# Optimization experiments

Hardware: AMD Instinct MI355X
Metric: run time of the kernel (lower is better)

## Reference

```python
import jax, jax.numpy as jnp
import numpy as np

VOXEL_SIZE = 0.4
PC_START = jnp.array([-75.2, -75.2], dtype=jnp.float32)
GAMMA = 1.1
RADII = (0.8, 1.6)
NSAMPLES = (16, 32)


def _sq_dist(a, b):
    # a:[N,3], b:[N,3] -> [N,N] squared distances (no [N,N,3] intermediate)
    sa = jnp.sum(a * a, axis=-1)
    sb = jnp.sum(b * b, axis=-1)
    return jnp.maximum(sa[:, None] + sb[None, :] - 2.0 * (a @ b.T), 0.0)


def _ball_group(d2, valid, pts, r, k):
    # CUDA ball_query semantics: first-k in-radius neighbor indices (index order),
    # empty slots padded with the first found index (0 if none).
    N = d2.shape[0]
    mask = (d2 < r * r) & valid[None, :]
    skey = jnp.where(mask, jnp.arange(N, dtype=jnp.int32)[None, :], N)
    idx = jnp.sort(skey, axis=-1)[:, :k]            # [N,k]
    first = idx[:, :1]
    idx = jnp.where(idx == N, first, idx)
    idx = jnp.where(idx == N, 0, idx)
    grouped_xyz = pts[idx, :3] - pts[:, None, :3]   # [N,k,3] relative xyz
    return jnp.concatenate([grouped_xyz, pts[idx, 3:5]], axis=-1)  # [N,k,5] (use_xyz)


def _mlp(x, ws, bs):
    for w, b in zip(ws, bs):
        x = jax.nn.relu(x @ w.T + b)
    return x


def _frame(pts, boxes, mlps, num_sample):
    # pts: [N,5] (x,y,z,intensity,time); boxes: [M,7]
    xy = pts[:, :2]
    coords = jnp.floor((xy - PC_START) / VOXEL_SIZE)              # per-point voxel xy coord
    qcoords = jnp.floor((boxes[:, :2] - PC_START) / VOXEL_SIZE)   # box voxel coords
    half_diag = jnp.linalg.norm(boxes[:, 3:5] * 0.5, axis=-1)
    rad_vox = jnp.ceil(half_diag * GAMMA / VOXEL_SIZE)
    dvox = jnp.abs(qcoords[:, None, :] - coords[None, :, :])      # [M,N,2]
    valid = jnp.any(jnp.all(dvox < rad_vox[:, None, None], axis=-1), axis=0)  # [N]

    # cylindrical_pool: per-box top-k points inside cylinder radius
    cur_radiis = half_diag * GAMMA
    dis = jnp.linalg.norm(boxes[:, None, :2] - xy[None, :, :], axis=-1)  # [M,N]
    point_mask = (dis <= cur_radiis[:, None]) & valid[None, :]
    sampled_mask, sampled_idx = jax.lax.top_k(point_mask.astype(pts.dtype), num_sample)

    # PointNet++ SA-MSG evaluated at every point (equivalent to unique->gather in torch src)
    d2 = _sq_dist(pts[:, :3], pts[:, :3])
    feats = [pts[:, :3]]  # use_absolute_xyz: concat query xyz first
    for r, k, (ws, bs) in zip(RADII, NSAMPLES, mlps):
        g = _ball_group(d2, valid, pts, r, k)
        feats.append(jnp.max(_mlp(g, ws, bs), axis=1))  # max-pool over neighbors
    feats = jnp.concatenate(feats, axis=-1)             # [N, 3+32+64]

    sampled_points = pts[sampled_idx] * sampled_mask[..., None]  # zero out-of-radius slots
    return sampled_points, feats[sampled_idx]


def _forward(points, trajectory_rois, params, num_sample):
    B, T, N, C = points.shape
    M = trajectory_rois.shape[2]
    sp, pf = jax.vmap(lambda p, b: _frame(p, b, params, num_sample))(
        points.reshape(B * T, N, C), trajectory_rois.reshape(B * T, M, -1))

    def _merge(x):
        x = x.reshape(B, T, M, num_sample, x.shape[-1])
        return x.transpose(0, 2, 1, 3, 4).reshape(B, M, T * num_sample, x.shape[-1])

    return _merge(sp), _merge(pf)


def setup_inputs():
    key = jax.random.key(0)
    ks = jax.random.split(key, 24)
    B, T, N, M = 2, 4, 4096, 128
    xy = jax.random.uniform(ks[0], (B, T, N, 2), minval=-74.0, maxval=74.0)
    z = jax.random.uniform(ks[1], (B, T, N, 1), minval=-2.0, maxval=4.0)
    inten = jax.random.uniform(ks[2], (B, T, N, 1))
    ts = jnp.broadcast_to(jnp.arange(T, dtype=jnp.float32)[None, :, None, None] * 0.1, (B, T, N, 1))
    points = jnp.concatenate([xy, z, inten, ts], axis=-1)
    bxy = jax.random.uniform(ks[3], (B, T, M, 2), minval=-70.0, maxval=70.0)
    bz = jax.random.uniform(ks[4], (B, T, M, 1), minval=-1.0, maxval=1.0)
    bdxy = jax.random.uniform(ks[5], (B, T, M, 2), minval=1.5, maxval=5.0)
    bdz = jax.random.uniform(ks[6], (B, T, M, 1), minval=1.0, maxval=2.0)
    bh = jax.random.uniform(ks[7], (B, T, M, 1), minval=0.0, maxval=6.28)
    trajectory_rois = jnp.concatenate([bxy, bz, bdxy, bdz, bh], axis=-1)
    inp = {"points": points, "trajectory_rois": trajectory_rois}
    dims = [("w00", 16, 5), ("w01", 16, 16), ("w02", 32, 16),
            ("w10", 32, 5), ("w11", 32, 32), ("w12", 64, 32)]
    for i, (nm, o, ic) in enumerate(dims):
        inp[nm] = jax.random.normal(ks[8 + i], (o, ic), dtype=jnp.float32) / np.sqrt(ic)
        inp["b" + nm[1:]] = jnp.zeros((o,), dtype=jnp.float32)
    inp["num_sample"] = 32
    return inp


def reference(points, trajectory_rois, w00, b00, w01, b01, w02, b02,
              w10, b10, w11, b11, w12, b12, num_sample):
    params = (((w00, w01, w02), (b00, b01, b02)),
              ((w10, w11, w12), (b10, b11, b12)))
    return _forward(points, trajectory_rois, params, num_sample)
```

## Files before the change

### kernel.cpp

```cpp
#include <hip/hip_runtime.h>
#include <hip/hip_bf16.h>
#include <stdint.h>

#define NFRM 8
#define NPTS 4096
#define NBOX 128
#define NS   32
#define TT   4
#define BB   2
#define FEATC 99
#define OUT1OFF (BB*NBOX*TT*NS*5)

#define WS_SPK    0u
#define WS_EPK    524288u
#define WS_FEATS  786432u
#define WS_SIDX   13762560u
#define WS_FLAGS  13893632u
#define WS_NCNT   14024704u
#define WS_NLST   14024736u
#define WS_VPK    14155808u
#define WS_VEK    14680096u
#define WS_VORIG  14942240u
#define WS_VCNT   15073312u
#define WS_WT     15073344u

__device__ __forceinline__ float rdl(float x, int l){
    return __int_as_float(__builtin_amdgcn_readlane(__float_as_int(x), l));
}

__global__ void k_wprep(const float* __restrict__ w00,const float* __restrict__ w01,
                        const float* __restrict__ w02,const float* __restrict__ w10,
                        const float* __restrict__ w11,const float* __restrict__ w12,
                        float* __restrict__ wt)
{
    int t = threadIdx.x;
    for (int idx=t; idx<80;   idx+=256){ int o=idx/5,  i=idx%5;  wt[      i*16+o]=w00[idx]; }
    for (int idx=t; idx<256;  idx+=256){ int o=idx/16, i=idx%16; wt[  80+ i*16+o]=w01[idx]; }
    for (int idx=t; idx<512;  idx+=256){ int o=idx/16, i=idx%16; wt[ 336+ i*32+o]=w02[idx]; }
    for (int idx=t; idx<160;  idx+=256){ int o=idx/5,  i=idx%5;  wt[ 848+ i*32+o]=w10[idx]; }
    for (int idx=t; idx<1024; idx+=256){ int o=idx/32, i=idx%32; wt[1008+ i*32+o]=w11[idx]; }
    for (int idx=t; idx<2048; idx+=256){ int o=idx/32, i=idx%32; wt[2032+ i*64+o]=w12[idx]; }
}

__global__ void k_prep(const float* __restrict__ pts, const float* __restrict__ rois,
                       float4* __restrict__ spk, float2* __restrict__ epk)
{
    int f = blockIdx.x >> 4;
    int n = ((blockIdx.x & 15) << 8) | threadIdx.x;
    __shared__ float bqx[NBOX], bqy[NBOX], brv[NBOX];
    if (threadIdx.x < NBOX){
        const float* bp = rois + (size_t)(f*NBOX + threadIdx.x)*7;
        float bx=bp[0], by=bp[1], dx=bp[3], dy=bp[4];
        float hx=__fmul_rn(dx,0.5f), hy=__fmul_rn(dy,0.5f);
        float hd=sqrtf(__fadd_rn(__fmul_rn(hx,hx),__fmul_rn(hy,hy)));
        brv[threadIdx.x]=ceilf(__fdiv_rn(__fmul_rn(hd,1.1f),0.4f));
        bqx[threadIdx.x]=floorf(__fdiv_rn(__fsub_rn(bx,-75.2f),0.4f));
        bqy[threadIdx.x]=floorf(__fdiv_rn(__fsub_rn(by,-75.2f),0.4f));
    }
    __syncthreads();
    const float* pp = pts + (size_t)(f*NPTS+n)*5;
    float x=pp[0], y=pp[1], z=pp[2], it=pp[3], ts=pp[4];
    float cx=floorf(__fdiv_rn(__fsub_rn(x,-75.2f),0.4f));
    float cy=floorf(__fdiv_rn(__fsub_rn(y,-75.2f),0.4f));
    float v=0.f;
    for (int m=0;m<NBOX;m++)
        if (fabsf(bqx[m]-cx)<brv[m] && fabsf(bqy[m]-cy)<brv[m]){ v=1.f; break; }
    spk[f*NPTS+n]=make_float4(x,y,z,v);
    epk[f*NPTS+n]=make_float2(it,ts);
}

__global__ __launch_bounds__(1024) void k_valid(
    const float4* __restrict__ spk, const float2* __restrict__ epk,
    float4* __restrict__ vpk, float2* __restrict__ vek,
    int* __restrict__ vorig, int* __restrict__ vcnt)
{
    int f = blockIdx.x;
    int tid = threadIdx.x, wv = tid >> 6, lane = tid & 63;
    __shared__ int wcnt[16];
    __shared__ int sbase;
    if (tid == 0) sbase = 0;
    __syncthreads();
    uint64_t below = (1ull<<lane)-1ull;
    for (int j0=0; j0<NPTS; j0+=1024){
        int j = j0 + tid;
        float4 q = spk[f*NPTS+j];
        float2 e = epk[f*NPTS+j];
        bool pred = q.w > 0.5f;
        uint64_t m = __ballot(pred);
        int lp = __popcll(m & below);
        if (lane == 0) wcnt[wv] = __popcll(m);
        __syncthreads();
        int off = sbase;
        for (int w=0; w<wv; w++) off += wcnt[w];
        if (pred){
            int pos = off + lp;
            float sb = __fadd_rn(__fadd_rn(__fmul_rn(q.x,q.x),__fmul_rn(q.y,q.y)),__fmul_rn(q.z,q.z));
            vpk[f*NPTS+pos] = make_float4(q.x,q.y,q.z,sb);
            vek[f*NPTS+pos] = e;
            vorig[f*NPTS+pos] = j;
        }
        __syncthreads();
        if (tid == 0){ int t=0; for (int w=0;w<16;w++) t+=wcnt[w]; sbase += t; }
        __syncthreads();
    }
    if (tid == 0) vcnt[f] = sbase;
}

__global__ void k_select(const float4* __restrict__ spk, const float2* __restrict__ epk,
                         const float4* __restrict__ vpk, const int* __restrict__ vorig,
                         const int* __restrict__ vcnt,
                         const float* __restrict__ rois, float* __restrict__ out,
                         int* __restrict__ sidx, int* __restrict__ flags)
{
    int id = blockIdx.x;
    int f = id >> 7, m = id & 127;
    int lane = threadIdx.x;
    const float* bp = rois + (size_t)(f*NBOX+m)*7;
    float bx=bp[0], by=bp[1], dx=bp[3], dy=bp[4];
    float hx=__fmul_rn(dx,0.5f), hy=__fmul_rn(dy,0.5f);
    float hd=sqrtf(__fadd_rn(__fmul_rn(hx,hx),__fmul_rn(hy,hy)));
    float rr=__fmul_rn(hd,1.1f);

    __shared__ int lt[32], lf[32];
    const float4* fsp = spk + f*NPTS;
    const float4* fvp = vpk + f*NPTS;
    const int*    fvo = vorig + f*NPTS;
    int vc = vcnt[f];
    uint64_t below = (1ull<<lane)-1ull;

    int cT=0;
    for (int v0=0; v0<vc; v0+=64){
        int vi = v0 + lane;
        int vic = min(vi, vc-1);
        float4 q = fvp[vic];
        float ddx=__fsub_rn(bx,q.x), ddy=__fsub_rn(by,q.y);
        float dis=sqrtf(__fadd_rn(__fmul_rn(ddx,ddx),__fmul_rn(ddy,ddy)));
        bool pm = (vi < vc) && (dis <= rr);
        uint64_t mT=__ballot(pm);
        if (pm){ int pos=cT+__popcll(mT&below); if (pos<32) lt[pos]=fvo[vic]; }
        cT += __popcll(mT);
        if (cT>=32) break;
    }
    int cF=0;
    for (int j0=0; j0<NPTS; j0+=64){
        int j=j0+lane;
        float4 q = fsp[j];
        float ddx=__fsub_rn(bx,q.x), ddy=__fsub_rn(by,q.y);
        float dis=sqrtf(__fadd_rn(__fmul_rn(ddx,ddx),__fmul_rn(ddy,ddy)));
        bool fl = !((dis <= rr) && (q.w > 0.5f));
        uint64_t mF=__ballot(fl);
        if (fl){ int pos=cF+__popcll(mF&below); if (pos<32) lf[pos]=j; }
        cF += __popcll(mF);
        if (cF>=32) break;
    }
    __syncthreads();
    cT = min(cT,32);
    if (lane < 32){
        int s = lane;
        bool masked = s < cT;
        int idx = masked ? lt[s] : lf[s-cT];
        float mk = masked ? 1.f : 0.f;
        sidx[(f*NBOX+m)*NS+s]=idx;
        flags[f*NPTS+idx]=1;
        int b = f >> 2, t = f & 3;
        size_t row = (((size_t)(b*NBOX+m))*TT + t)*NS + s;
        float4 q = fsp[idx]; float2 e = epk[f*NPTS+idx];
        float* o0 = out + row*5;
        o0[0]=q.x*mk; o0[1]=q.y*mk; o0[2]=q.z*mk; o0[3]=e.x*mk; o0[4]=e.y*mk;
    }
}

__global__ void k_compact(const int* __restrict__ flags, int* __restrict__ gcnt,
                          int* __restrict__ glist)
{
    int f = blockIdx.x >> 3;
    int seg = blockIdx.x & 7;
    int tid = threadIdx.x, lane = tid & 63;
    uint64_t below = (1ull<<lane)-1ull;
    for (int i0 = seg*512; i0 < seg*512+512; i0 += 256){
        int i = i0 + tid;
        bool fl = flags[f*NPTS+i] != 0;
        uint64_t m = __ballot(fl);
        int cnt = __popcll(m);
        if (cnt){
            int base = 0;
            if (lane == 0) base = atomicAdd(gcnt, cnt);
            base = __shfl(base, 0);
            if (fl) glist[base + __popcll(m & below)] = (f<<12) | i;
        }
    }
}

__global__ __launch_bounds__(256) void k_mlp(
    const float4* __restrict__ spk, const float2* __restrict__ epk,
    const float4* __restrict__ vpk, const float2* __restrict__ vek,
    const int* __restrict__ vcnt,
    const int* __restrict__ gcntp, const int* __restrict__ glist,
    float* __restrict__ feats, const float* __restrict__ wt,
    const float* __restrict__ b00,const float* __restrict__ b01,
    const float* __restrict__ b02,const float* __restrict__ b10,
    const float* __restrict__ b11,const float* __restrict__ b12)
{
    int gcnt = *gcntp;
    if ((int)blockIdx.x * 4 >= gcnt) return;
    int tid = threadIdx.x;
    int wv = tid >> 6, lane = tid & 63;
    __shared__ int lists[4][48];
    int* l1 = lists[wv];
    int* l2 = lists[wv]+16;

    float wr00[5], wr01[16], wr02[16], wr10[5], wr11[32], wr12[32];
    float br00=0.f, br01=0.f, br02=0.f, br10=0.f, br11=0.f, br12=0.f;
    #pragma unroll
    for (int i=0;i<5;i++){ wr00[i]=0.f; wr10[i]=0.f; }
    #pragma unroll
    for (int i=0;i<16;i++){ wr01[i]=0.f; wr02[i]=0.f; }
    #pragma unroll
    for (int i=0;i<32;i++){ wr11[i]=0.f; wr12[i]=0.f; }
    if (lane < 16){
        #pragma unroll
        for (int i=0;i<5;i++)  wr00[i]=wt[i*16+lane];
        br00=b00[lane];
        #pragma unroll
        for (int i=0;i<16;i++) wr01[i]=wt[80+i*16+lane];
        br01=b01[lane];
    }
    if (lane < 32){
        #pragma unroll
        for (int i=0;i<16;i++) wr02[i]=wt[336+i*32+lane];
        br02=b02[lane];
        #pragma unroll
        for (int i=0;i<5;i++)  wr10[i]=wt[848+i*32+lane];
        br10=b10[lane];
        #pragma unroll
        for (int i=0;i<32;i++) wr11[i]=wt[1008+i*32+lane];
        br11=b11[lane];
    }
    #pragma unroll
    for (int i=0;i<32;i++) wr12[i]=wt[2032+i*64+lane];
    br12=b12[lane];

    const float RR1 = (float)(0.8*0.8);
    const float RR2 = (float)(1.6*1.6);
    uint64_t below = (1ull<<lane)-1ull;

    for (int li = blockIdx.x*4 + wv; li < gcnt; li += 8192){
        int pe = glist[li];
        int f = pe >> 12, n = pe & 4095;
        const float4* fsp = spk + f*NPTS;
        const float2* fep = epk + f*NPTS;
        const float4* fvp = vpk + f*NPTS;
        const float2* fve = vek + f*NPTS;
        int vc = vcnt[f];
        float4 me = fsp[n];
        float sa = __fadd_rn(__fadd_rn(__fmul_rn(me.x,me.x),__fmul_rn(me.y,me.y)),__fmul_rn(me.z,me.z));

        int cnt1=0, cnt2=0;
        for (int v0=0; v0<vc; v0+=64){
            int vi = v0 + lane;
            int vic = min(vi, vc-1);
            float4 q = fvp[vic];
            float dot = __fadd_rn(__fadd_rn(__fmul_rn(me.x,q.x),__fmul_rn(me.y,q.y)),__fmul_rn(me.z,q.z));
            float d2 = fmaxf(__fsub_rn(__fadd_rn(sa,q.w),__fmul_rn(2.0f,dot)), 0.f);
            bool inb = (vi < vc);
            bool p1 = inb && (d2 < RR1);
            bool p2 = inb && (d2 < RR2);
            uint64_t m1 = __ballot(p1), m2 = __ballot(p2);
            if (p1){ int pos = cnt1 + __popcll(m1 & below); if (pos < 16) l1[pos] = vi; }
            if (p2){ int pos = cnt2 + __popcll(m2 & below); if (pos < 32) l2[pos] = vi; }
            cnt1 += __popcll(m1); cnt2 += __popcll(m2);
            if (cnt1 >= 16 && cnt2 >= 32) break;
        }
        cnt1 = min(cnt1,16); cnt2 = min(cnt2,32);

        float* fo = feats + (size_t)(f*NPTS+n)*FEATC;
        float4 q0 = fsp[0]; float2 e0 = fep[0];

        {
            float pmax = 0.f;
            #pragma unroll 1
            for (int kb=0; kb<16; kb+=4){
                float4 qb[4]; float2 eb[4];
                #pragma unroll
                for (int j=0;j<4;j++){
                    int kk = kb+j;
                    int vi = (cnt1>0) ? ((kk<cnt1)? l1[kk] : l1[0]) : -1;
                    if (vi >= 0){ qb[j]=fvp[vi]; eb[j]=fve[vi]; }
                    else        { qb[j]=q0;      eb[j]=e0; }
                }
                float h1[4];
                #pragma unroll
                for (int j=0;j<4;j++){
                    float a1 = br00;
                    a1 += __fsub_rn(qb[j].x,me.x)*wr00[0];
                    a1 += __fsub_rn(qb[j].y,me.y)*wr00[1];
                    a1 += __fsub_rn(qb[j].z,me.z)*wr00[2];
                    a1 += eb[j].x*wr00[3];
                    a1 += eb[j].y*wr00[4];
                    h1[j] = fmaxf(a1,0.f);
                }
                float a2[4] = {br01,br01,br01,br01};
                #pragma unroll
                for (int c=0;c<16;c++){
                    #pragma unroll
                    for (int j=0;j<4;j++) a2[j] += rdl(h1[j],c)*wr01[c];
                }
                float h2[4];
                #pragma unroll
                for (int j=0;j<4;j++) h2[j] = fmaxf(a2[j],0.f);
                float a3[4] = {br02,br02,br02,br02};
                #pragma unroll
                for (int c=0;c<16;c++){
                    #pragma unroll
                    for (int j=0;j<4;j++) a3[j] += rdl(h2[j],c)*wr02[c];
                }
                #pragma unroll
                for (int j=0;j<4;j++) pmax = fmaxf(pmax, fmaxf(a3[j],0.f));
            }
            if (lane < 3){
                float mv = (lane==0)? me.x : ((lane==1)? me.y : me.z);
                fo[lane] = mv;
            }
            if (lane < 32) fo[3+lane] = pmax;
        }

        {
            float pmax = 0.f;
            #pragma unroll 1
            for (int kb=0; kb<32; kb+=4){
                float4 qb[4]; float2 eb[4];
                #pragma unroll
                for (int j=0;j<4;j++){
                    int kk = kb+j;
                    int vi = (cnt2>0) ? ((kk<cnt2)? l2[kk] : l2[0]) : -1;
                    if (vi >= 0){ qb[j]=fvp[vi]; eb[j]=fve[vi]; }
                    else        { qb[j]=q0;      eb[j]=e0; }
                }
                float h1[4];
                #pragma unroll
                for (int j=0;j<4;j++){
                    float a1 = br10;
                    a1 += __fsub_rn(qb[j].x,me.x)*wr10[0];
                    a1 += __fsub_rn(qb[j].y,me.y)*wr10[1];
                    a1 += __fsub_rn(qb[j].z,me.z)*wr10[2];
                    a1 += eb[j].x*wr10[3];
                    a1 += eb[j].y*wr10[4];
                    h1[j] = fmaxf(a1,0.f);
                }
                float a2[4] = {br11,br11,br11,br11};
                #pragma unroll
                for (int c=0;c<32;c++){
                    #pragma unroll
                    for (int j=0;j<4;j++) a2[j] += rdl(h1[j],c)*wr11[c];
                }
                float h2[4];
                #pragma unroll
                for (int j=0;j<4;j++) h2[j] = fmaxf(a2[j],0.f);
                float a3[4] = {br12,br12,br12,br12};
                #pragma unroll
                for (int c=0;c<32;c++){
                    #pragma unroll
                    for (int j=0;j<4;j++) a3[j] += rdl(h2[j],c)*wr12[c];
                }
                #pragma unroll
                for (int j=0;j<4;j++) pmax = fmaxf(pmax, fmaxf(a3[j],0.f));
            }
            fo[35+lane] = pmax;
        }
    }
}

__global__ void k_gather(const float* __restrict__ feats, const int* __restrict__ sidx,
                         float* __restrict__ out)
{
    int id = blockIdx.x;
    int f = id >> 7, m = id & 127;
    int tid = threadIdx.x;
    int s = tid >> 3, j = tid & 7;
    int idx = sidx[(f*NBOX+m)*NS+s];
    int b = f >> 2, t = f & 3;
    size_t row = (((size_t)(b*NBOX+m))*TT + t)*NS + s;
    const float* fi = feats + (size_t)(f*NPTS+idx)*FEATC;
    float* o1 = out + OUT1OFF + row*FEATC;
    for (int c=j; c<FEATC; c+=8) o1[c]=fi[c];
}

extern "C" void kernel_launch(void* const* d_in, const int* in_sizes, int n_in,
                              void* d_out, int out_size, void* d_ws, size_t ws_size,
                              hipStream_t stream)
{
    const float* pts  = (const float*)d_in[0];
    const float* rois = (const float*)d_in[1];
    const float* w00=(const float*)d_in[2],  *b00=(const float*)d_in[3];
    const float* w01=(const float*)d_in[4],  *b01=(const float*)d_in[5];
    const float* w02=(const float*)d_in[6],  *b02=(const float*)d_in[7];
    const float* w10=(const float*)d_in[8],  *b10=(const float*)d_in[9];
    const float* w11=(const float*)d_in[10], *b11=(const float*)d_in[11];
    const float* w12=(const float*)d_in[12], *b12=(const float*)d_in[13];
    float* out = (float*)d_out;

    char* ws = (char*)d_ws;
    float4* spk   = (float4*)(ws + WS_SPK);
    float2* epk   = (float2*)(ws + WS_EPK);
    float*  feats = (float*) (ws + WS_FEATS);
    int*    sidx  = (int*)   (ws + WS_SIDX);
    int*    flags = (int*)   (ws + WS_FLAGS);
    int*    gcnt  = (int*)   (ws + WS_NCNT);
    int*    glist = (int*)   (ws + WS_NLST);
    float4* vpk   = (float4*)(ws + WS_VPK);
    float2* vek   = (float2*)(ws + WS_VEK);
    int*    vorig = (int*)   (ws + WS_VORIG);
    int*    vcnt  = (int*)   (ws + WS_VCNT);
    float*  wtr   = (float*) (ws + WS_WT);

    hipMemsetAsync(ws + WS_FLAGS, 0, (WS_NCNT - WS_FLAGS) + 32, stream);

    hipLaunchKernelGGL(k_wprep,  dim3(1), dim3(256), 0, stream,
                       w00, w01, w02, w10, w11, w12, wtr);
    hipLaunchKernelGGL(k_prep,   dim3(NFRM*16), dim3(256), 0, stream, pts, rois, spk, epk);
    hipLaunchKernelGGL(k_valid,  dim3(NFRM), dim3(1024), 0, stream, spk, epk, vpk, vek, vorig, vcnt);
    hipLaunchKernelGGL(k_select, dim3(NFRM*NBOX), dim3(64), 0, stream,
                       spk, epk, vpk, vorig, vcnt, rois, out, sidx, flags);
    hipLaunchKernelGGL(k_compact, dim3(64), dim3(256), 0, stream, flags, gcnt, glist);
    hipLaunchKernelGGL(k_mlp,    dim3(2048), dim3(256), 0, stream,
                       spk, epk, vpk, vek, vcnt, gcnt, glist, feats, wtr,
                       b00,b01,b02,b10,b11,b12);
    hipLaunchKernelGGL(k_gather, dim3(NFRM*NBOX), dim3(256), 0, stream,
                       feats, sidx, out);
}
```

Measured before the change: 118.1 us.

## Fuse weight prep, flag clearing and compaction into neighbouring kernels

Weight transposition and counter reset move into an extra block of k_prep, flag zeroing moves into k_prep, and the hipMemset is dropped. The separate k_compact pass is replaced by atomicExch-based dedup inside k_select that appends fresh indices to the global list directly. The in-radius scan in k_select is also unrolled to load two 64-point chunks at once. This removes three launches/dispatches at the cost of more atomics and a nondeterministic glist order.

Result: faster. 109.2 us (-7.5%).

```diff
diff --git a/kernel.cpp b/kernel.cpp
--- a/kernel.cpp
+++ b/kernel.cpp
@@ -28,23 +28,25 @@
     return __int_as_float(__builtin_amdgcn_readlane(__float_as_int(x), l));
 }
 
-__global__ void k_wprep(const float* __restrict__ w00,const float* __restrict__ w01,
-                        const float* __restrict__ w02,const float* __restrict__ w10,
-                        const float* __restrict__ w11,const float* __restrict__ w12,
-                        float* __restrict__ wt)
-{
-    int t = threadIdx.x;
-    for (int idx=t; idx<80;   idx+=256){ int o=idx/5,  i=idx%5;  wt[      i*16+o]=w00[idx]; }
-    for (int idx=t; idx<256;  idx+=256){ int o=idx/16, i=idx%16; wt[  80+ i*16+o]=w01[idx]; }
-    for (int idx=t; idx<512;  idx+=256){ int o=idx/16, i=idx%16; wt[ 336+ i*32+o]=w02[idx]; }
-    for (int idx=t; idx<160;  idx+=256){ int o=idx/5,  i=idx%5;  wt[ 848+ i*32+o]=w10[idx]; }
-    for (int idx=t; idx<1024; idx+=256){ int o=idx/32, i=idx%32; wt[1008+ i*32+o]=w11[idx]; }
-    for (int idx=t; idx<2048; idx+=256){ int o=idx/32, i=idx%32; wt[2032+ i*64+o]=w12[idx]; }
-}
-
 __global__ void k_prep(const float* __restrict__ pts, const float* __restrict__ rois,
-                       float4* __restrict__ spk, float2* __restrict__ epk)
-{
+                       float4* __restrict__ spk, float2* __restrict__ epk,
+                       const float* __restrict__ w00,const float* __restrict__ w01,
+                       const float* __restrict__ w02,const float* __restrict__ w10,
+                       const float* __restrict__ w11,const float* __restrict__ w12,
+                       float* __restrict__ wt, int* __restrict__ flags,
+                       int* __restrict__ gcnt)
+{
+    if (blockIdx.x == 128){
+        int t = threadIdx.x;
+        if (t == 0) *gcnt = 0;
+        for (int idx=t; idx<80;   idx+=256){ int o=idx/5,  i=idx%5;  wt[      i*16+o]=w00[idx]; }
+        for (int idx=t; idx<256;  idx+=256){ int o=idx/16, i=idx%16; wt[  80+ i*16+o]=w01[idx]; }
+        for (int idx=t; idx<512;  idx+=256){ int o=idx/16, i=idx%16; wt[ 336+ i*32+o]=w02[idx]; }
+        for (int idx=t; idx<160;  idx+=256){ int o=idx/5,  i=idx%5;  wt[ 848+ i*32+o]=w10[idx]; }
+        for (int idx=t; idx<1024; idx+=256){ int o=idx/32, i=idx%32; wt[1008+ i*32+o]=w11[idx]; }
+        for (int idx=t; idx<2048; idx+=256){ int o=idx/32, i=idx%32; wt[2032+ i*64+o]=w12[idx]; }
+        return;
+    }
     int f = blockIdx.x >> 4;
     int n = ((blockIdx.x & 15) << 8) | threadIdx.x;
     __shared__ float bqx[NBOX], bqy[NBOX], brv[NBOX];
@@ -57,6 +59,7 @@
         bqx[threadIdx.x]=floorf(__fdiv_rn(__fsub_rn(bx,-75.2f),0.4f));
         bqy[threadIdx.x]=floorf(__fdiv_rn(__fsub_rn(by,-75.2f),0.4f));
     }
+    flags[f*NPTS+n] = 0;
     __syncthreads();
     const float* pp = pts + (size_t)(f*NPTS+n)*5;
     float x=pp[0], y=pp[1], z=pp[2], it=pp[3], ts=pp[4];
@@ -110,7 +113,8 @@
                          const float4* __restrict__ vpk, const int* __restrict__ vorig,
                          const int* __restrict__ vcnt,
                          const float* __restrict__ rois, float* __restrict__ out,
-                         int* __restrict__ sidx, int* __restrict__ flags)
+                         int* __restrict__ sidx, int* __restrict__ flags,
+                         int* __restrict__ gcnt, int* __restrict__ glist)
 {
     int id = blockIdx.x;
     int f = id >> 7, m = id & 127;
@@ -129,17 +133,31 @@
     uint64_t below = (1ull<<lane)-1ull;
 
     int cT=0;
-    for (int v0=0; v0<vc; v0+=64){
-        int vi = v0 + lane;
-        int vic = min(vi, vc-1);
-        float4 q = fvp[vic];
-        float ddx=__fsub_rn(bx,q.x), ddy=__fsub_rn(by,q.y);
-        float dis=sqrtf(__fadd_rn(__fmul_rn(ddx,ddx),__fmul_rn(ddy,ddy)));
-        bool pm = (vi < vc) && (dis <= rr);
-        uint64_t mT=__ballot(pm);
-        if (pm){ int pos=cT+__popcll(mT&below); if (pos<32) lt[pos]=fvo[vic]; }
-        cT += __popcll(mT);
-        if (cT>=32) break;
+    for (int v0=0; v0<vc; v0+=128){
+        int viA = v0 + lane;
+        int viB = v0 + 64 + lane;
+        int vicA = min(viA, vc-1);
+        int vicB = min(viB, vc-1);
+        float4 qA = fvp[vicA];
+        float4 qB = fvp[vicB];
+        {
+            float ddx=__fsub_rn(bx,qA.x), ddy=__fsub_rn(by,qA.y);
+            float dis=sqrtf(__fadd_rn(__fmul_rn(ddx,ddx),__fmul_rn(ddy,ddy)));
+            bool pm = (viA < vc) && (dis <= rr);
+            uint64_t mT=__ballot(pm);
+            if (pm){ int pos=cT+__popcll(mT&below); if (pos<32) lt[pos]=fvo[vicA]; }
+            cT += __popcll(mT);
+            if (cT>=32) break;
+        }
+        if (v0 + 64 < vc){
+            float ddx=__fsub_rn(bx,qB.x), ddy=__fsub_rn(by,qB.y);
+            float dis=sqrtf(__fadd_rn(__fmul_rn(ddx,ddx),__fmul_rn(ddy,ddy)));
+            bool pm = (viB < vc) && (dis <= rr);
+            uint64_t mT=__ballot(pm);
+            if (pm){ int pos=cT+__popcll(mT&below); if (pos<32) lt[pos]=fvo[vicB]; }
+            cT += __popcll(mT);
+            if (cT>=32) break;
+        }
     }
     int cF=0;
     for (int j0=0; j0<NPTS; j0+=64){
@@ -161,32 +179,20 @@
         int idx = masked ? lt[s] : lf[s-cT];
         float mk = masked ? 1.f : 0.f;
         sidx[(f*NBOX+m)*NS+s]=idx;
-        flags[f*NPTS+idx]=1;
         int b = f >> 2, t = f & 3;
         size_t row = (((size_t)(b*NBOX+m))*TT + t)*NS + s;
         float4 q = fsp[idx]; float2 e = epk[f*NPTS+idx];
         float* o0 = out + row*5;
         o0[0]=q.x*mk; o0[1]=q.y*mk; o0[2]=q.z*mk; o0[3]=e.x*mk; o0[4]=e.y*mk;
-    }
-}
-
-__global__ void k_compact(const int* __restrict__ flags, int* __restrict__ gcnt,
-                          int* __restrict__ glist)
-{
-    int f = blockIdx.x >> 3;
-    int seg = blockIdx.x & 7;
-    int tid = threadIdx.x, lane = tid & 63;
-    uint64_t below = (1ull<<lane)-1ull;
-    for (int i0 = seg*512; i0 < seg*512+512; i0 += 256){
-        int i = i0 + tid;
-        bool fl = flags[f*NPTS+i] != 0;
-        uint64_t m = __ballot(fl);
-        int cnt = __popcll(m);
-        if (cnt){
+        int old = atomicExch(&flags[f*NPTS+idx], 1);
+        bool fresh = (old == 0);
+        uint64_t mm = __ballot(fresh);
+        if (fresh){
+            int ldr = __ffsll((unsigned long long)mm) - 1;
             int base = 0;
-            if (lane == 0) base = atomicAdd(gcnt, cnt);
-            base = __shfl(base, 0);
-            if (fl) glist[base + __popcll(m & below)] = (f<<12) | i;
+            if (lane == ldr) base = atomicAdd(gcnt, __popcll(mm));
+            base = __shfl(base, ldr);
+            glist[base + __popcll(mm & below)] = (f<<12) | idx;
         }
     }
 }
@@ -413,15 +419,11 @@
     int*    vcnt  = (int*)   (ws + WS_VCNT);
     float*  wtr   = (float*) (ws + WS_WT);
 
-    hipMemsetAsync(ws + WS_FLAGS, 0, (WS_NCNT - WS_FLAGS) + 32, stream);
-
-    hipLaunchKernelGGL(k_wprep,  dim3(1), dim3(256), 0, stream,
-                       w00, w01, w02, w10, w11, w12, wtr);
-    hipLaunchKernelGGL(k_prep,   dim3(NFRM*16), dim3(256), 0, stream, pts, rois, spk, epk);
+    hipLaunchKernelGGL(k_prep,   dim3(NFRM*16+1), dim3(256), 0, stream,
+                       pts, rois, spk, epk, w00,w01,w02,w10,w11,w12, wtr, flags, gcnt);
     hipLaunchKernelGGL(k_valid,  dim3(NFRM), dim3(1024), 0, stream, spk, epk, vpk, vek, vorig, vcnt);
     hipLaunchKernelGGL(k_select, dim3(NFRM*NBOX), dim3(64), 0, stream,
-                       spk, epk, vpk, vorig, vcnt, rois, out, sidx, flags);
-    hipLaunchKernelGGL(k_compact, dim3(64), dim3(256), 0, stream, flags, gcnt, glist);
+                       spk, epk, vpk, vorig, vcnt, rois, out, sidx, flags, gcnt, glist);
     hipLaunchKernelGGL(k_mlp,    dim3(2048), dim3(256), 0, stream,
                        spk, epk, vpk, vek, vcnt, gcnt, glist, feats, wtr,
                        b00,b01,b02,b10,b11,b12);
```
